# Optimization experiments

Measured on AMD Instinct MI355X. Metric: run time of the kernel, lower is better.

Reference implementation:

```python
import jax
import jax.numpy as jnp
from jax import lax
import numpy as np

SLIDING_WINDOW_LEN = 192
EPS = 1e-6


def setup_inputs() -> dict:
    key = jax.random.key(0)
    X = jax.random.normal(key, (8, 8, 257, 2000), dtype=jnp.float32)
    return {"X": X, "ref_channel": 0}


def _forgetting_normalization(XrMag):
    # XrMag: [B, 1, F, T] magnitude of reference channel
    alpha = (SLIDING_WINDOW_LEN - 1) / (SLIDING_WINDOW_LEN + 1)
    # mean over frequency, keepdim -> [B, 1, 1, T]
    XrMM = XrMag.mean(axis=2, keepdims=True)
    T = XrMM.shape[-1]
    t = jnp.arange(T, dtype=XrMM.dtype)
    # original: alpha_this = min((t-1)/(t+1), alpha) for t < L, else alpha;
    # since (t-1)/(t+1) >= alpha for t >= L, a single minimum is exact.
    a = jnp.minimum((t - 1.0) / (t + 1.0), alpha)  # [T]

    x_seq = jnp.moveaxis(XrMM, -1, 0)  # [T, B, 1, 1]
    mu0 = jnp.zeros_like(x_seq[0])

    def step(mu, inp):
        a_t, x_t = inp
        mu = a_t * mu + (1.0 - a_t) * x_t
        return mu, mu

    _, mus = lax.scan(step, mu0, (a, x_seq))  # [T, B, 1, 1]
    return jnp.moveaxis(mus, 0, -1)  # [B, 1, 1, T]


def reference(X, ref_channel):
    # X: [B, C, F, T] (real stand-in for complex); ref_channel: python int
    Xr = X[:, ref_channel:ref_channel + 1]  # [B, 1, F, T]
    XrMag = jnp.abs(Xr)
    # original detaches XrMM (.detach().cpu()) -> stop_gradient
    XrMM = lax.stop_gradient(_forgetting_normalization(XrMag)) + EPS  # [B,1,1,T]
    X_norm = X / XrMM  # broadcast over C, F
    return X_norm
```

## Files before the change

### kernel.cpp

```cpp
#include <hip/hip_runtime.h>

#define B_N 8
#define C_N 8
#define F_N 257
#define T_N 2000
#define EPSF 1e-6f

#define FCH 32
#define FPC 9

typedef float f32x4 __attribute__((ext_vector_type(4)));

__global__ __launch_bounds__(512) void partial_mean_kernel(
    const float* __restrict__ X, const int* __restrict__ ref_ch,
    f32x4* __restrict__ part4 )
{
    const int b   = blockIdx.x;
    const int c   = blockIdx.y;
    const int tid = threadIdx.x;
    if (tid >= T_N / 4) return;

    const int rc = ref_ch[0];
    const f32x4* Xb4 =
        (const f32x4*)(X + ((size_t)(b * C_N + rc)) * (size_t)F_N * T_N);

    const int f0 = c * FPC;
    const int f1 = (f0 + FPC < F_N) ? (f0 + FPC) : F_N;

    f32x4 acc = {0.f, 0.f, 0.f, 0.f};
    for (int f = f0; f < f1; ++f) {
        f32x4 v = Xb4[f * (T_N / 4) + tid];
        acc.x += fabsf(v.x); acc.y += fabsf(v.y);
        acc.z += fabsf(v.z); acc.w += fabsf(v.w);
    }
    part4[(b * FCH + c) * (T_N / 4) + tid] = acc;
}

__global__ __launch_bounds__(512) void scan_kernel(
    const f32x4* __restrict__ part4,
    f32x4* __restrict__ inv4 )
{
    __shared__ float s_mean[T_N];
    __shared__ float s_wA[8];
    __shared__ float s_wB[8];
    const float ALPHA = (float)(191.0 / 193.0);

    const int b   = blockIdx.x;
    const int tid = threadIdx.x;

    if (tid < T_N / 4) {
        f32x4 s = {0.f, 0.f, 0.f, 0.f};
        #pragma unroll
        for (int c = 0; c < FCH; ++c)
            s += part4[(b * FCH + c) * (T_N / 4) + tid];
        const int t = tid * 4;
        const float inv_f = 1.f / (float)F_N;
        s_mean[t + 0] = s.x * inv_f;
        s_mean[t + 1] = s.y * inv_f;
        s_mean[t + 2] = s.z * inv_f;
        s_mean[t + 3] = s.w * inv_f;
    }
    __syncthreads();

    float A = 1.f, Bv = 0.f;
    const int tbase = tid * 4;
    #pragma unroll
    for (int k = 0; k < 4; ++k) {
        const int t = tbase + k;
        if (t < T_N) {
            const float tf = (float)t;
            const float a = fminf((tf - 1.f) / (tf + 1.f), ALPHA);
            const float x = s_mean[t];
            Bv = a * Bv + (1.f - a) * x;
            A  = a * A;
        }
    }

    const int lane = tid & 63;
    #pragma unroll
    for (int d = 1; d < 64; d <<= 1) {
        const float pA = __shfl_up(A, d);
        const float pB = __shfl_up(Bv, d);
        if (lane >= d) {
            Bv = A * pB + Bv;
            A  = A * pA;
        }
    }

    const int wid = tid >> 6;
    if (lane == 63) { s_wA[wid] = A; s_wB[wid] = Bv; }
    __syncthreads();
    if (tid == 0) {
        float cA = 1.f, cB = 0.f;
        #pragma unroll
        for (int w = 0; w < 8; ++w) {
            const float nA = s_wA[w] * cA;
            const float nB = s_wA[w] * cB + s_wB[w];
            s_wA[w] = cA; s_wB[w] = cB;
            cA = nA; cB = nB;
        }
    }
    __syncthreads();

    float eA = __shfl_up(A, 1);
    float eB = __shfl_up(Bv, 1);
    if (lane == 0) { eA = 1.f; eB = 0.f; }
    float mu = eA * s_wB[wid] + eB;

    if (tid < T_N / 4) {
        f32x4 r;
        #pragma unroll
        for (int k = 0; k < 4; ++k) {
            const int t = tbase + k;
            const float tf = (float)t;
            const float a = fminf((tf - 1.f) / (tf + 1.f), ALPHA);
            const float x = s_mean[t];
            mu = a * mu + (1.f - a) * x;
            r[k] = 1.f / (mu + EPSF);
        }
        inv4[b * (T_N / 4) + tid] = r;
    }
}

__global__ __launch_bounds__(256) void norm_kernel(
    const f32x4* __restrict__ X4,
    const f32x4* __restrict__ inv4,
    f32x4* __restrict__ out4)
{
    const int PER_B = C_N * F_N * T_N / 4;
    const int i  = blockIdx.x * 256 + threadIdx.x;
    if (i >= PER_B) return;
    const int b  = blockIdx.y;
    const int tq = i % (T_N / 4);

    const size_t g = (size_t)b * PER_B + i;
    const f32x4 iv = inv4[b * (T_N / 4) + tq];
    const f32x4 x  = __builtin_nontemporal_load(X4 + g);
    __builtin_nontemporal_store(x * iv, out4 + g);
}

extern "C" void kernel_launch(void* const* d_in, const int* in_sizes, int n_in,
                              void* d_out, int out_size, void* d_ws, size_t ws_size,
                              hipStream_t stream) {
    const float* X  = (const float*)d_in[0];
    const int*   rc = (const int*)d_in[1];

    float* inv  = (float*)d_ws;
    float* part = (float*)d_ws + B_N * T_N;

    dim3 gA(B_N, FCH);
    partial_mean_kernel<<<gA, 512, 0, stream>>>(X, rc, (f32x4*)part);

    scan_kernel<<<B_N, 512, 0, stream>>>((const f32x4*)part, (f32x4*)inv);

    const int PER_B = C_N * F_N * T_N / 4;
    dim3 gC((PER_B + 255) / 256, B_N);
    norm_kernel<<<gC, 256, 0, stream>>>(
        (const f32x4*)X, (const f32x4*)inv, (f32x4*)d_out);
}
```

Baseline: 56.86 us.

## Fuse mean, scan and normalization into one cooperative persistent kernel

Replaces the three-kernel pipeline with a single cooperative kernel of 512 blocks, using two grid syncs between the partial abs-sum, the per-timestep reduction and a per-block redundant scan. Each block then normalizes a strided slice using inverse means held in shared memory. The aim is to remove two launch gaps and global round trips for the inverse means. In exchange it adds grid-wide barriers, recomputes the scan in all 64 blocks per batch, and drops the nontemporal load/store hints. The old three-kernel path remains as a fallback.

```diff
diff --git a/kernel.cpp b/kernel.cpp
--- a/kernel.cpp
+++ b/kernel.cpp
@@ -1,64 +1,181 @@
 #include <hip/hip_runtime.h>
+#include <hip/hip_cooperative_groups.h>
+
+namespace cg = cooperative_groups;
 
 #define B_N 8
 #define C_N 8
 #define F_N 257
 #define T_N 2000
+#define TQ_N (T_N / 4)
 #define EPSF 1e-6f
 
 #define FCH 32
 #define FPC 9
+#define GBLK 512
+#define BPB  64
+#define NTHR 512
+#define PER_B (C_N * F_N * TQ_N)
+#define STRIDE (BPB * NTHR)
 
 typedef float f32x4 __attribute__((ext_vector_type(4)));
+
+__global__ __launch_bounds__(NTHR, 4) void fused_kernel(
+    const float* __restrict__ X, const int* __restrict__ ref_ch,
+    f32x4* __restrict__ part4 ,
+    f32x4* __restrict__ mean4 ,
+    f32x4* __restrict__ out4)
+{
+    cg::grid_group grid = cg::this_grid();
+    __shared__ f32x4 s_inv4[TQ_N];
+    __shared__ float s_wA[8];
+    __shared__ float s_wB[8];
+
+    const int bid = blockIdx.x;
+    const int tid = threadIdx.x;
+    const int b   = bid >> 6;
+    const int c6  = bid & 63;
+
+    if (c6 < FCH && tid < TQ_N) {
+        const int rc = ref_ch[0];
+        const f32x4* Xb4 =
+            (const f32x4*)(X + ((size_t)(b * C_N + rc)) * (size_t)F_N * T_N);
+        const int f0 = c6 * FPC;
+        const int f1 = (f0 + FPC < F_N) ? (f0 + FPC) : F_N;
+        f32x4 acc = {0.f, 0.f, 0.f, 0.f};
+        for (int f = f0; f < f1; ++f) {
+            f32x4 v = Xb4[f * TQ_N + tid];
+            acc.x += fabsf(v.x); acc.y += fabsf(v.y);
+            acc.z += fabsf(v.z); acc.w += fabsf(v.w);
+        }
+        part4[(b * FCH + c6) * TQ_N + tid] = acc;
+    }
+    grid.sync();
+
+    if (tid < 256) {
+        const int ql = tid >> 5;
+        const int c  = tid & 31;
+        const int q  = c6 * 8 + ql;
+        if (q < TQ_N) {
+            f32x4 v = part4[(b * FCH + c) * TQ_N + q];
+            #pragma unroll
+            for (int d = 16; d >= 1; d >>= 1) {
+                v.x += __shfl_xor(v.x, d);
+                v.y += __shfl_xor(v.y, d);
+                v.z += __shfl_xor(v.z, d);
+                v.w += __shfl_xor(v.w, d);
+            }
+            if (c == 0) mean4[b * TQ_N + q] = v * (1.f / (float)F_N);
+        }
+    }
+    grid.sync();
+
+    const float ALPHA = (float)(191.0 / 193.0);
+    f32x4 m = {0.f, 0.f, 0.f, 0.f};
+    if (tid < TQ_N) m = mean4[b * TQ_N + tid];
+
+    float A = 1.f, Bv = 0.f;
+    const int tbase = tid * 4;
+    if (tid < TQ_N) {
+        #pragma unroll
+        for (int k = 0; k < 4; ++k) {
+            const float tf = (float)(tbase + k);
+            const float a  = fminf((tf - 1.f) / (tf + 1.f), ALPHA);
+            Bv = a * Bv + (1.f - a) * m[k];
+            A  = a * A;
+        }
+    }
+    const int lane = tid & 63;
+    #pragma unroll
+    for (int d = 1; d < 64; d <<= 1) {
+        const float pA = __shfl_up(A, d);
+        const float pB = __shfl_up(Bv, d);
+        if (lane >= d) { Bv = A * pB + Bv; A = A * pA; }
+    }
+    const int wid = tid >> 6;
+    if (lane == 63) { s_wA[wid] = A; s_wB[wid] = Bv; }
+    __syncthreads();
+    if (tid == 0) {
+        float cA = 1.f, cB = 0.f;
+        #pragma unroll
+        for (int w = 0; w < 8; ++w) {
+            const float nA = s_wA[w] * cA;
+            const float nB = s_wA[w] * cB + s_wB[w];
+            s_wA[w] = cA; s_wB[w] = cB;
+            cA = nA; cB = nB;
+        }
+    }
+    __syncthreads();
+    float eA = __shfl_up(A, 1);
+    float eB = __shfl_up(Bv, 1);
+    if (lane == 0) { eA = 1.f; eB = 0.f; }
+    float mu = eA * s_wB[wid] + eB;
+
+    if (tid < TQ_N) {
+        f32x4 r;
+        #pragma unroll
+        for (int k = 0; k < 4; ++k) {
+            const float tf = (float)(tbase + k);
+            const float a  = fminf((tf - 1.f) / (tf + 1.f), ALPHA);
+            mu = a * mu + (1.f - a) * m[k];
+            r[k] = 1.f / (mu + EPSF);
+        }
+        s_inv4[tid] = r;
+    }
+    __syncthreads();
+
+    const f32x4* Xb = (const f32x4*)X + (size_t)b * PER_B;
+    f32x4*       Ob = out4 + (size_t)b * PER_B;
+
+    int i  = c6 * NTHR + tid;
+    int tq = i % TQ_N;
+    const int DT = STRIDE % TQ_N;
+    #pragma unroll 4
+    for (int it = 0; it < 31; ++it) {
+        Ob[i] = Xb[i] * s_inv4[tq];
+        i += STRIDE;
+        tq += DT; if (tq >= TQ_N) tq -= TQ_N;
+    }
+    if (i < PER_B) Ob[i] = Xb[i] * s_inv4[tq];
+}
 
 __global__ __launch_bounds__(512) void partial_mean_kernel(
     const float* __restrict__ X, const int* __restrict__ ref_ch,
-    f32x4* __restrict__ part4 )
-{
-    const int b   = blockIdx.x;
-    const int c   = blockIdx.y;
-    const int tid = threadIdx.x;
-    if (tid >= T_N / 4) return;
-
+    f32x4* __restrict__ part4)
+{
+    const int b = blockIdx.x, c = blockIdx.y, tid = threadIdx.x;
+    if (tid >= TQ_N) return;
     const int rc = ref_ch[0];
     const f32x4* Xb4 =
         (const f32x4*)(X + ((size_t)(b * C_N + rc)) * (size_t)F_N * T_N);
-
     const int f0 = c * FPC;
     const int f1 = (f0 + FPC < F_N) ? (f0 + FPC) : F_N;
-
     f32x4 acc = {0.f, 0.f, 0.f, 0.f};
     for (int f = f0; f < f1; ++f) {
-        f32x4 v = Xb4[f * (T_N / 4) + tid];
+        f32x4 v = Xb4[f * TQ_N + tid];
         acc.x += fabsf(v.x); acc.y += fabsf(v.y);
         acc.z += fabsf(v.z); acc.w += fabsf(v.w);
     }
-    part4[(b * FCH + c) * (T_N / 4) + tid] = acc;
+    part4[(b * FCH + c) * TQ_N + tid] = acc;
 }
 
 __global__ __launch_bounds__(512) void scan_kernel(
-    const f32x4* __restrict__ part4,
-    f32x4* __restrict__ inv4 )
+    const f32x4* __restrict__ part4, f32x4* __restrict__ inv4)
 {
     __shared__ float s_mean[T_N];
     __shared__ float s_wA[8];
     __shared__ float s_wB[8];
     const float ALPHA = (float)(191.0 / 193.0);
-
-    const int b   = blockIdx.x;
-    const int tid = threadIdx.x;
-
-    if (tid < T_N / 4) {
+    const int b = blockIdx.x, tid = threadIdx.x;
+
+    if (tid < TQ_N) {
         f32x4 s = {0.f, 0.f, 0.f, 0.f};
         #pragma unroll
-        for (int c = 0; c < FCH; ++c)
-            s += part4[(b * FCH + c) * (T_N / 4) + tid];
+        for (int c = 0; c < FCH; ++c) s += part4[(b * FCH + c) * TQ_N + tid];
         const int t = tid * 4;
         const float inv_f = 1.f / (float)F_N;
-        s_mean[t + 0] = s.x * inv_f;
-        s_mean[t + 1] = s.y * inv_f;
-        s_mean[t + 2] = s.z * inv_f;
-        s_mean[t + 3] = s.w * inv_f;
+        s_mean[t + 0] = s.x * inv_f; s_mean[t + 1] = s.y * inv_f;
+        s_mean[t + 2] = s.z * inv_f; s_mean[t + 3] = s.w * inv_f;
     }
     __syncthreads();
 
@@ -70,23 +187,17 @@
         if (t < T_N) {
             const float tf = (float)t;
             const float a = fminf((tf - 1.f) / (tf + 1.f), ALPHA);
-            const float x = s_mean[t];
-            Bv = a * Bv + (1.f - a) * x;
+            Bv = a * Bv + (1.f - a) * s_mean[t];
             A  = a * A;
         }
     }
-
     const int lane = tid & 63;
     #pragma unroll
     for (int d = 1; d < 64; d <<= 1) {
         const float pA = __shfl_up(A, d);
         const float pB = __shfl_up(Bv, d);
-        if (lane >= d) {
-            Bv = A * pB + Bv;
-            A  = A * pA;
-        }
-    }
-
+        if (lane >= d) { Bv = A * pB + Bv; A = A * pA; }
+    }
     const int wid = tid >> 6;
     if (lane == 63) { s_wA[wid] = A; s_wB[wid] = Bv; }
     __syncthreads();
@@ -101,42 +212,35 @@
         }
     }
     __syncthreads();
-
     float eA = __shfl_up(A, 1);
     float eB = __shfl_up(Bv, 1);
     if (lane == 0) { eA = 1.f; eB = 0.f; }
     float mu = eA * s_wB[wid] + eB;
 
-    if (tid < T_N / 4) {
+    if (tid < TQ_N) {
         f32x4 r;
         #pragma unroll
         for (int k = 0; k < 4; ++k) {
             const int t = tbase + k;
             const float tf = (float)t;
             const float a = fminf((tf - 1.f) / (tf + 1.f), ALPHA);
-            const float x = s_mean[t];
-            mu = a * mu + (1.f - a) * x;
+            mu = a * mu + (1.f - a) * s_mean[t];
             r[k] = 1.f / (mu + EPSF);
         }
-        inv4[b * (T_N / 4) + tid] = r;
+        inv4[b * TQ_N + tid] = r;
     }
 }
 
 __global__ __launch_bounds__(256) void norm_kernel(
-    const f32x4* __restrict__ X4,
-    const f32x4* __restrict__ inv4,
+    const f32x4* __restrict__ X4, const f32x4* __restrict__ inv4,
     f32x4* __restrict__ out4)
 {
-    const int PER_B = C_N * F_N * T_N / 4;
-    const int i  = blockIdx.x * 256 + threadIdx.x;
+    const int i = blockIdx.x * 256 + threadIdx.x;
     if (i >= PER_B) return;
     const int b  = blockIdx.y;
-    const int tq = i % (T_N / 4);
-
+    const int tq = i % TQ_N;
     const size_t g = (size_t)b * PER_B + i;
-    const f32x4 iv = inv4[b * (T_N / 4) + tq];
-    const f32x4 x  = __builtin_nontemporal_load(X4 + g);
-    __builtin_nontemporal_store(x * iv, out4 + g);
+    out4[g] = X4[g] * inv4[b * TQ_N + tq];
 }
 
 extern "C" void kernel_launch(void* const* d_in, const int* in_sizes, int n_in,
@@ -145,16 +249,26 @@
     const float* X  = (const float*)d_in[0];
     const int*   rc = (const int*)d_in[1];
 
-    float* inv  = (float*)d_ws;
-    float* part = (float*)d_ws + B_N * T_N;
+    f32x4* part = (f32x4*)d_ws;
+    f32x4* mean = part + B_N * FCH * TQ_N;
+    f32x4* out  = (f32x4*)d_out;
+
+    int nb = 0;
+    hipError_t qe = hipOccupancyMaxActiveBlocksPerMultiprocessor(
+        &nb, fused_kernel, NTHR, 0);
+    bool coop_ok = (qe == hipSuccess) && (nb * 256 >= GBLK);
+
+    if (coop_ok) {
+        void* args[5] = {(void*)&X, (void*)&rc, (void*)&part,
+                         (void*)&mean, (void*)&out};
+        hipError_t le = hipLaunchCooperativeKernel(
+            fused_kernel, dim3(GBLK), dim3(NTHR), args, 0, stream);
+        if (le == hipSuccess) return;
+    }
 
     dim3 gA(B_N, FCH);
-    partial_mean_kernel<<<gA, 512, 0, stream>>>(X, rc, (f32x4*)part);
-
-    scan_kernel<<<B_N, 512, 0, stream>>>((const f32x4*)part, (f32x4*)inv);
-
-    const int PER_B = C_N * F_N * T_N / 4;
+    partial_mean_kernel<<<gA, 512, 0, stream>>>(X, rc, part);
+    scan_kernel<<<B_N, 512, 0, stream>>>(part, mean);
     dim3 gC((PER_B + 255) / 256, B_N);
-    norm_kernel<<<gC, 256, 0, stream>>>(
-        (const f32x4*)X, (const f32x4*)inv, (f32x4*)d_out);
-}
+    norm_kernel<<<gC, 256, 0, stream>>>((const f32x4*)X, mean, out);
+}
```

New measurement: 173.7 us. 3.06x slower.
